# Optimization experiments

Measured on AMD Instinct MI355X. Metric: run time of the kernel, lower is better.

Reference implementation:

```python
import jax, jax.numpy as jnp
import numpy as np

N = 1000000
E = 16000000


def gcn_conv(x, W, b, src, dst, dinv_sqrt):
    # x: [N, Cin]; W: [Cin, Cout]; src/dst: [E'] (self-loops included)
    xw = x @ W                                   # [N, Cout]
    norm = dinv_sqrt[src] * dinv_sqrt[dst]       # [E']
    msg = xw[src] * norm[:, None]                # [E', Cout]
    out = jax.ops.segment_sum(msg, dst, num_segments=x.shape[0])
    return out + b


def setup_inputs() -> dict:
    key = jax.random.key(0)
    ks = jax.random.split(key, 8)
    x = jax.random.normal(ks[0], (N, 1), dtype=jnp.float32)
    edge_index = jax.random.randint(ks[1], (2, E), 0, N, dtype=jnp.int64)
    W1 = jax.random.normal(ks[2], (1, 3), dtype=jnp.float32)
    b1 = jax.random.normal(ks[3], (3,), dtype=jnp.float32) * 0.1
    W2 = jax.random.normal(ks[4], (3, 3), dtype=jnp.float32) * 0.5
    b2 = jax.random.normal(ks[5], (3,), dtype=jnp.float32) * 0.1
    W3 = jax.random.normal(ks[6], (3, 3), dtype=jnp.float32) * 0.5
    b3 = jax.random.normal(ks[7], (3,), dtype=jnp.float32) * 0.1
    return {"x": x, "edge_index": edge_index, "W1": W1, "b1": b1,
            "W2": W2, "b2": b2, "W3": W3, "b3": b3}


def reference(x, edge_index, W1, b1, W2, b2, W3, b3):
    n = x.shape[0]
    # add self-loops (PyG GCNConv default)
    loop = jnp.arange(n, dtype=edge_index.dtype)
    src = jnp.concatenate([edge_index[0], loop])
    dst = jnp.concatenate([edge_index[1], loop])
    # symmetric normalization: deg over targets of A + I
    deg = jax.ops.segment_sum(jnp.ones_like(dst, dtype=x.dtype), dst, num_segments=n)
    dinv_sqrt = jnp.where(deg > 0, jax.lax.rsqrt(deg), 0.0)
    h = jax.nn.relu(gcn_conv(x, W1, b1, src, dst, dinv_sqrt))
    h = jax.nn.relu(gcn_conv(h, W2, b2, src, dst, dinv_sqrt))
    h = jax.nn.relu(gcn_conv(h, W3, b3, src, dst, dinv_sqrt))
    return h
```

## Files before the change

kernel.cpp:

```cpp
#include <hip/hip_runtime.h>

#define THREADS 256
#define TILE 8192
#define TPB_S 512
#define EPT 16
#define BUCKET_BITS 10
#define BUCKET_SIZE 1024
#define NT_MAX 2048
#define STAGE_CAP 15616
#define MSK 0xFFFFFu

__device__ __forceinline__ long long llmin(long long a, long long b) { return a < b ? a : b; }


__global__ void detect_i64_kernel(const int* __restrict__ e, int* __restrict__ flag) {
    if (blockIdx.x == 0 && threadIdx.x == 0) {
        bool all_odd_zero = true, any_even = false;
#pragma unroll
        for (int k = 0; k < 16; ++k) {
            if (e[2 * k + 1] != 0) all_odd_zero = false;
            if (e[2 * k] != 0) any_even = true;
        }
        *flag = (all_odd_zero && any_even) ? 1 : 0;
    }
}


__global__ __launch_bounds__(TPB_S) void binsort_kernel(
        const int* __restrict__ e, long long E, const int* __restrict__ flag,
        int nbuck, int* __restrict__ packed, int* __restrict__ ofs) {
    __shared__ int hist[1024];
    __shared__ int sarr[TPB_S];
    __shared__ int srec[TILE];
    const int tid = threadIdx.x;
    hist[tid] = 0;
    hist[tid + TPB_S] = 0;
    __syncthreads();

    const bool i64 = (*flag != 0);
    const long long beg = (long long)blockIdx.x * TILE;
    const int tile_len = (int)llmin((long long)TILE, E - beg);

    int rec[EPT];
    int bkt[EPT];
#pragma unroll
    for (int k = 0; k < EPT; ++k) {
        int j = tid + k * TPB_S;
        bkt[k] = -1;
        if (j < tile_len) {
            long long idx = beg + j;
            int s, d;
            if (i64) { s = ((const int2*)e)[idx].x; d = ((const int2*)e)[E + idx].x; }
            else     { s = e[idx];                  d = e[E + idx]; }
            bkt[k] = d >> BUCKET_BITS;
            rec[k] = ((d & (BUCKET_SIZE - 1)) << 20) | s;
            atomicAdd(&hist[bkt[k]], 1);
        }
    }
    __syncthreads();

    int v0 = hist[2 * tid], v1 = hist[2 * tid + 1];
    sarr[tid] = v0 + v1;
    __syncthreads();
    for (int off = 1; off < TPB_S; off <<= 1) {
        int t = (tid >= off) ? sarr[tid - off] : 0;
        __syncthreads();
        sarr[tid] += t;
        __syncthreads();
    }
    int excl = (tid == 0) ? 0 : sarr[tid - 1];
    hist[2 * tid] = excl;
    hist[2 * tid + 1] = excl + v0;
    __syncthreads();

    int* orow = ofs + (size_t)blockIdx.x * nbuck;
    if (tid < nbuck) orow[tid] = hist[tid];
    if (tid + TPB_S < nbuck) orow[tid + TPB_S] = hist[tid + TPB_S];
    __syncthreads();

#pragma unroll
    for (int k = 0; k < EPT; ++k) {
        if (bkt[k] >= 0) {
            int pos = atomicAdd(&hist[bkt[k]], 1);
            srec[pos] = rec[k];
        }
    }
    __syncthreads();

    int* prow = packed + (size_t)blockIdx.x * TILE;
    for (int j = tid; j < tile_len; j += TPB_S) prow[j] = srec[j];
}

#define TRT 32
__global__ void transpose_kernel(const int* __restrict__ in, int rows, int cols,
                                 int* __restrict__ outT) {
    __shared__ int tb[TRT][TRT + 1];
    int c0 = blockIdx.x * TRT, r0 = blockIdx.y * TRT;
    int lx = threadIdx.x, ly = threadIdx.y;
    for (int dy = ly; dy < TRT; dy += 8) {
        int r = r0 + dy, c = c0 + lx;
        if (r < rows && c < cols) tb[dy][lx] = in[(size_t)r * cols + c];
    }
    __syncthreads();
    for (int dy = ly; dy < TRT; dy += 8) {
        int r = c0 + dy, c = r0 + lx;
        if (r < cols && c < rows) outT[(size_t)r * rows + c] = tb[lx][dy];
    }
}


__global__ __launch_bounds__(THREADS) void bcnt_kernel(
        const int* __restrict__ ofsT, long long E, int ntiles, int nbuck,
        int* __restrict__ bcnt) {
    __shared__ int sh[THREADS];
    const int b = blockIdx.x, tid = threadIdx.x;
    const int* row0 = ofsT + (size_t)b * ntiles;
    const int* row1 = row0 + ntiles;
    const bool last_b = (b == nbuck - 1);
    int s = 0;
    for (int t = tid; t < ntiles; t += THREADS) {
        int o = row0[t];
        int tl = (t == ntiles - 1) ? (int)(E - (long long)t * TILE) : TILE;
        int o2 = last_b ? tl : row1[t];
        s += o2 - o;
    }
    sh[tid] = s;
    __syncthreads();
    for (int off = THREADS >> 1; off > 0; off >>= 1) {
        if (tid < off) sh[tid] += sh[tid + off];
        __syncthreads();
    }
    if (tid == 0) bcnt[b] = sh[0];
}

__global__ __launch_bounds__(1024) void bscan_kernel(
        const int* __restrict__ bcnt, int nbuck, int* __restrict__ bs) {
    __shared__ int sh[1024];
    int tid = threadIdx.x;
    int v = (tid < nbuck) ? bcnt[tid] : 0;
    sh[tid] = v;
    __syncthreads();
    for (int off = 1; off < 1024; off <<= 1) {
        int t = (tid >= off) ? sh[tid - off] : 0;
        __syncthreads();
        sh[tid] += t;
        __syncthreads();
    }
    if (tid < nbuck) bs[tid] = sh[tid] - v;
    if (tid == nbuck - 1) bs[nbuck] = sh[tid];
}


__global__ __launch_bounds__(TPB_S) void merge_kernel(
        const int* __restrict__ ofsT, const int* __restrict__ packed,
        const int* __restrict__ bs, long long E, int ntiles, int nbuck,
        const float* __restrict__ x,
        int* __restrict__ merged, float* __restrict__ dinv, float* __restrict__ p,
        int N) {
    __shared__ int lofs[NT_MAX];
    __shared__ int tsum[TPB_S];
    __shared__ int stage[STAGE_CAP];
    __shared__ int cnt[BUCKET_SIZE];
    const int tid = threadIdx.x, b = blockIdx.x;
    const int* row0 = ofsT + (size_t)b * ntiles;
    const int* row1 = row0 + ntiles;
    const bool last_b = (b == nbuck - 1);
    const int per = (ntiles + TPB_S - 1) / TPB_S;
    const int t0 = tid * per;

    for (int k = tid; k < BUCKET_SIZE; k += TPB_S) cnt[k] = 0;

    int s = 0;
    for (int k = 0; k < per; ++k) {
        int t = t0 + k;
        if (t < ntiles) {
            int o = row0[t];
            int tl = (t == ntiles - 1) ? (int)(E - (long long)t * TILE) : TILE;
            int o2 = last_b ? tl : row1[t];
            lofs[t] = s;
            s += o2 - o;
        }
    }
    tsum[tid] = s;
    __syncthreads();
    for (int off = 1; off < TPB_S; off <<= 1) {
        int t = (tid >= off) ? tsum[tid - off] : 0;
        __syncthreads();
        tsum[tid] += t;
        __syncthreads();
    }
    const int excl = tsum[tid] - s;
    const int total = tsum[TPB_S - 1];
    for (int k = 0; k < per; ++k) {
        int t = t0 + k;
        if (t < ntiles) lofs[t] += excl;
    }
    __syncthreads();

    const int bsb = bs[b];
    for (int k = 0; k < per; ++k) {
        int t = t0 + k;
        if (t >= ntiles) break;
        int o = row0[t];
        int tl = (t == ntiles - 1) ? (int)(E - (long long)t * TILE) : TILE;
        int o2 = last_b ? tl : row1[t];
        const int* pr = packed + (size_t)t * TILE;
        int q = lofs[t];
        int j = o;
        for (; j + 4 <= o2; j += 4, q += 4) {
            int a0 = pr[j], a1 = pr[j + 1], a2 = pr[j + 2], a3 = pr[j + 3];
            atomicAdd(&cnt[((unsigned)a0) >> 20], 1);
            atomicAdd(&cnt[((unsigned)a1) >> 20], 1);
            atomicAdd(&cnt[((unsigned)a2) >> 20], 1);
            atomicAdd(&cnt[((unsigned)a3) >> 20], 1);
            if (q + 3 < STAGE_CAP) {
                stage[q] = a0; stage[q + 1] = a1; stage[q + 2] = a2; stage[q + 3] = a3;
            } else {
                if (q < STAGE_CAP) stage[q] = a0; else merged[bsb + q] = a0;
                if (q + 1 < STAGE_CAP) stage[q + 1] = a1; else merged[bsb + q + 1] = a1;
                if (q + 2 < STAGE_CAP) stage[q + 2] = a2; else merged[bsb + q + 2] = a2;
                merged[bsb + q + 3] = a3;
            }
        }
        for (; j < o2; ++j, ++q) {
            int a0 = pr[j];
            atomicAdd(&cnt[((unsigned)a0) >> 20], 1);
            if (q < STAGE_CAP) stage[q] = a0; else merged[bsb + q] = a0;
        }
    }
    __syncthreads();

    const int wlen = total < STAGE_CAP ? total : STAGE_CAP;
    for (int j = tid; j < wlen; j += TPB_S) merged[bsb + j] = stage[j];

    int nbase = b << BUCKET_BITS;
    for (int j = tid; j < BUCKET_SIZE; j += TPB_S) {
        int i = nbase + j;
        if (i < N) {
            float di = rsqrtf((float)cnt[j] + 1.0f);
            dinv[i] = di;
            p[i] = x[i] * di;
        }
    }
}


__global__ void layer1_bucket_kernel(const int* __restrict__ bs, const int* __restrict__ packed,
                                     const float* __restrict__ p, const float* __restrict__ dinv,
                                     const float* __restrict__ W1, const float* __restrict__ b1,
                                     const float* __restrict__ W2,
                                     float4* __restrict__ y2, int N) {
    __shared__ float acc[BUCKET_SIZE];
    for (int k = threadIdx.x; k < BUCKET_SIZE; k += blockDim.x) acc[k] = 0.0f;
    __syncthreads();
    int beg = bs[blockIdx.x], end = bs[blockIdx.x + 1];
    int stride = blockDim.x;
    int k = beg + threadIdx.x;
    for (; k + 3 * stride < end; k += 4 * stride) {
        unsigned r0 = packed[k], r1 = packed[k + stride];
        unsigned r2 = packed[k + 2 * stride], r3 = packed[k + 3 * stride];
        float v0 = p[r0 & MSK], v1 = p[r1 & MSK];
        float v2 = p[r2 & MSK], v3 = p[r3 & MSK];
        atomicAdd(&acc[r0 >> 20], v0);
        atomicAdd(&acc[r1 >> 20], v1);
        atomicAdd(&acc[r2 >> 20], v2);
        atomicAdd(&acc[r3 >> 20], v3);
    }
    for (; k < end; k += stride) {
        unsigned rec = (unsigned)packed[k];
        atomicAdd(&acc[rec >> 20], p[rec & MSK]);
    }
    __syncthreads();
    int base = blockIdx.x << BUCKET_BITS;
    for (int j = threadIdx.x; j < BUCKET_SIZE; j += blockDim.x) {
        int i = base + j;
        if (i >= N) continue;
        float di = dinv[i];
        float t = di * (acc[j] + p[i]);
        float h0 = fmaxf(t * W1[0] + b1[0], 0.0f);
        float h1 = fmaxf(t * W1[1] + b1[1], 0.0f);
        float h2 = fmaxf(t * W1[2] + b1[2], 0.0f);
        float4 o;
        o.x = di * (h0 * W2[0] + h1 * W2[3] + h2 * W2[6]);
        o.y = di * (h0 * W2[1] + h1 * W2[4] + h2 * W2[7]);
        o.z = di * (h0 * W2[2] + h1 * W2[5] + h2 * W2[8]);
        o.w = 0.0f;
        y2[i] = o;
    }
}

__global__ void layer_mid_bucket_kernel(const int* __restrict__ bs, const int* __restrict__ packed,
                                        const float4* __restrict__ y, const float* __restrict__ dinv,
                                        const float* __restrict__ b, const float* __restrict__ Wn,
                                        float4* __restrict__ ynext, int N) {
    __shared__ float acc[BUCKET_SIZE * 3];
    for (int k = threadIdx.x; k < BUCKET_SIZE * 3; k += blockDim.x) acc[k] = 0.0f;
    __syncthreads();
    int beg = bs[blockIdx.x], end = bs[blockIdx.x + 1];
    int stride = blockDim.x;
    int k = beg + threadIdx.x;
    for (; k + 3 * stride < end; k += 4 * stride) {
        unsigned r0 = packed[k], r1 = packed[k + stride];
        unsigned r2 = packed[k + 2 * stride], r3 = packed[k + 3 * stride];
        float4 v0 = y[r0 & MSK], v1 = y[r1 & MSK];
        float4 v2 = y[r2 & MSK], v3 = y[r3 & MSK];
        int d0 = (r0 >> 20) * 3, d1 = (r1 >> 20) * 3, d2 = (r2 >> 20) * 3, d3 = (r3 >> 20) * 3;
        atomicAdd(&acc[d0 + 0], v0.x); atomicAdd(&acc[d0 + 1], v0.y); atomicAdd(&acc[d0 + 2], v0.z);
        atomicAdd(&acc[d1 + 0], v1.x); atomicAdd(&acc[d1 + 1], v1.y); atomicAdd(&acc[d1 + 2], v1.z);
        atomicAdd(&acc[d2 + 0], v2.x); atomicAdd(&acc[d2 + 1], v2.y); atomicAdd(&acc[d2 + 2], v2.z);
        atomicAdd(&acc[d3 + 0], v3.x); atomicAdd(&acc[d3 + 1], v3.y); atomicAdd(&acc[d3 + 2], v3.z);
    }
    for (; k < end; k += stride) {
        unsigned rec = (unsigned)packed[k];
        float4 v = y[rec & MSK];
        int dl = (rec >> 20) * 3;
        atomicAdd(&acc[dl + 0], v.x);
        atomicAdd(&acc[dl + 1], v.y);
        atomicAdd(&acc[dl + 2], v.z);
    }
    __syncthreads();
    int base = blockIdx.x << BUCKET_BITS;
    for (int j = threadIdx.x; j < BUCKET_SIZE; j += blockDim.x) {
        int i = base + j;
        if (i >= N) continue;
        float di = dinv[i];
        float4 yi = y[i];
        float h0 = fmaxf(di * (acc[j * 3 + 0] + yi.x) + b[0], 0.0f);
        float h1 = fmaxf(di * (acc[j * 3 + 1] + yi.y) + b[1], 0.0f);
        float h2 = fmaxf(di * (acc[j * 3 + 2] + yi.z) + b[2], 0.0f);
        float4 o;
        o.x = di * (h0 * Wn[0] + h1 * Wn[3] + h2 * Wn[6]);
        o.y = di * (h0 * Wn[1] + h1 * Wn[4] + h2 * Wn[7]);
        o.z = di * (h0 * Wn[2] + h1 * Wn[5] + h2 * Wn[8]);
        o.w = 0.0f;
        ynext[i] = o;
    }
}

__global__ void layer_last_bucket_kernel(const int* __restrict__ bs, const int* __restrict__ packed,
                                         const float4* __restrict__ y, const float* __restrict__ dinv,
                                         const float* __restrict__ b,
                                         float* __restrict__ out, int N) {
    __shared__ float acc[BUCKET_SIZE * 3];
    for (int k = threadIdx.x; k < BUCKET_SIZE * 3; k += blockDim.x) acc[k] = 0.0f;
    __syncthreads();
    int beg = bs[blockIdx.x], end = bs[blockIdx.x + 1];
    int stride = blockDim.x;
    int k = beg + threadIdx.x;
    for (; k + 3 * stride < end; k += 4 * stride) {
        unsigned r0 = packed[k], r1 = packed[k + stride];
        unsigned r2 = packed[k + 2 * stride], r3 = packed[k + 3 * stride];
        float4 v0 = y[r0 & MSK], v1 = y[r1 & MSK];
        float4 v2 = y[r2 & MSK], v3 = y[r3 & MSK];
        int d0 = (r0 >> 20) * 3, d1 = (r1 >> 20) * 3, d2 = (r2 >> 20) * 3, d3 = (r3 >> 20) * 3;
        atomicAdd(&acc[d0 + 0], v0.x); atomicAdd(&acc[d0 + 1], v0.y); atomicAdd(&acc[d0 + 2], v0.z);
        atomicAdd(&acc[d1 + 0], v1.x); atomicAdd(&acc[d1 + 1], v1.y); atomicAdd(&acc[d1 + 2], v1.z);
        atomicAdd(&acc[d2 + 0], v2.x); atomicAdd(&acc[d2 + 1], v2.y); atomicAdd(&acc[d2 + 2], v2.z);
        atomicAdd(&acc[d3 + 0], v3.x); atomicAdd(&acc[d3 + 1], v3.y); atomicAdd(&acc[d3 + 2], v3.z);
    }
    for (; k < end; k += stride) {
        unsigned rec = (unsigned)packed[k];
        float4 v = y[rec & MSK];
        int dl = (rec >> 20) * 3;
        atomicAdd(&acc[dl + 0], v.x);
        atomicAdd(&acc[dl + 1], v.y);
        atomicAdd(&acc[dl + 2], v.z);
    }
    __syncthreads();
    int base = blockIdx.x << BUCKET_BITS;
    for (int j = threadIdx.x; j < BUCKET_SIZE; j += blockDim.x) {
        int i = base + j;
        if (i >= N) continue;
        float di = dinv[i];
        float4 yi = y[i];
        out[i * 3 + 0] = fmaxf(di * (acc[j * 3 + 0] + yi.x) + b[0], 0.0f);
        out[i * 3 + 1] = fmaxf(di * (acc[j * 3 + 1] + yi.y) + b[1], 0.0f);
        out[i * 3 + 2] = fmaxf(di * (acc[j * 3 + 2] + yi.z) + b[2], 0.0f);
    }
}


__global__ void deg_kernel(const int* __restrict__ e, long long E,
                           const int* __restrict__ flag, float* __restrict__ deg) {
    const bool i64 = (*flag != 0);
    long long i = (long long)blockIdx.x * blockDim.x + threadIdx.x;
    const long long stride = (long long)gridDim.x * blockDim.x;
    for (; i < E; i += stride) {
        long long t = i64 ? (long long)e[2 * E + 2 * i] : (long long)e[E + i];
        atomicAdd(deg + t, 1.0f);
    }
}

__global__ void node_init_kernel(const float* __restrict__ x, const float* __restrict__ W1,
                                 float* __restrict__ deg_dinv, float* __restrict__ A, int N) {
    int i = blockIdx.x * blockDim.x + threadIdx.x;
    if (i >= N) return;
    float di = rsqrtf(deg_dinv[i] + 1.0f);
    deg_dinv[i] = di;
    float v = x[i] * di;
    A[i * 3 + 0] = v * W1[0];
    A[i * 3 + 1] = v * W1[1];
    A[i * 3 + 2] = v * W1[2];
}

__global__ void scatter_kernel(const int* __restrict__ e, long long E,
                               const int* __restrict__ flag,
                               const float* __restrict__ y, float* __restrict__ acc) {
    const bool i64 = (*flag != 0);
    long long i = (long long)blockIdx.x * blockDim.x + threadIdx.x;
    const long long stride = (long long)gridDim.x * blockDim.x;
    for (; i < E; i += stride) {
        int s, t;
        if (i64) { s = e[2 * i]; t = e[2 * E + 2 * i]; }
        else     { s = e[i];     t = e[E + i]; }
        atomicAdd(acc + (long long)t * 3 + 0, y[(long long)s * 3 + 0]);
        atomicAdd(acc + (long long)t * 3 + 1, y[(long long)s * 3 + 1]);
        atomicAdd(acc + (long long)t * 3 + 2, y[(long long)s * 3 + 2]);
    }
}

__global__ void finalize_mid_kernel(const float* __restrict__ dinv, const float* __restrict__ y,
                                    float* __restrict__ acc, const float* __restrict__ b,
                                    const float* __restrict__ Wn, int N) {
    int i = blockIdx.x * blockDim.x + threadIdx.x;
    if (i >= N) return;
    float di = dinv[i];
    float h0 = fmaxf(di * (acc[i * 3 + 0] + y[i * 3 + 0]) + b[0], 0.0f);
    float h1 = fmaxf(di * (acc[i * 3 + 1] + y[i * 3 + 1]) + b[1], 0.0f);
    float h2 = fmaxf(di * (acc[i * 3 + 2] + y[i * 3 + 2]) + b[2], 0.0f);
    float z0 = di * (h0 * Wn[0] + h1 * Wn[3] + h2 * Wn[6]);
    float z1 = di * (h0 * Wn[1] + h1 * Wn[4] + h2 * Wn[7]);
    float z2 = di * (h0 * Wn[2] + h1 * Wn[5] + h2 * Wn[8]);
    acc[i * 3 + 0] = z0;
    acc[i * 3 + 1] = z1;
    acc[i * 3 + 2] = z2;
}

__global__ void finalize_last_kernel(const float* __restrict__ dinv, const float* __restrict__ y,
                                     const float* __restrict__ acc, const float* __restrict__ b,
                                     float* __restrict__ out, int N) {
    int i = blockIdx.x * blockDim.x + threadIdx.x;
    if (i >= N) return;
    float di = dinv[i];
    out[i * 3 + 0] = fmaxf(di * (acc[i * 3 + 0] + y[i * 3 + 0]) + b[0], 0.0f);
    out[i * 3 + 1] = fmaxf(di * (acc[i * 3 + 1] + y[i * 3 + 1]) + b[1], 0.0f);
    out[i * 3 + 2] = fmaxf(di * (acc[i * 3 + 2] + y[i * 3 + 2]) + b[2], 0.0f);
}


extern "C" void kernel_launch(void* const* d_in, const int* in_sizes, int n_in,
                              void* d_out, int out_size, void* d_ws, size_t ws_size,
                              hipStream_t stream) {
    const float* x  = (const float*)d_in[0];
    const int*   ei = (const int*)d_in[1];
    const float* W1 = (const float*)d_in[2];
    const float* b1 = (const float*)d_in[3];
    const float* W2 = (const float*)d_in[4];
    const float* b2 = (const float*)d_in[5];
    const float* W3 = (const float*)d_in[6];
    const float* b3 = (const float*)d_in[7];
    float* out = (float*)d_out;

    const long long N = in_sizes[0];
    const long long E = (long long)in_sizes[1] / 2;

    const int nbuck  = (int)((N + BUCKET_SIZE - 1) >> BUCKET_BITS);
    const int ntiles = (int)((E + TILE - 1) / TILE);

    char* w = (char*)d_ws;
    size_t off = 0;
    auto alloc = [&](size_t bytes) -> char* {
        char* pp = w + off;
        off = (off + bytes + 255) & ~(size_t)255;
        return pp;
    };

    int*    flag   = (int*)alloc(4);
    int*    ofs    = (int*)alloc((size_t)ntiles * nbuck * 4);
    int*    ofsT   = (int*)alloc((size_t)nbuck * ntiles * 4);
    int*    bcnt   = (int*)alloc((size_t)nbuck * 4);
    int*    bs     = (int*)alloc(((size_t)nbuck + 1) * 4);
    int*    packed = (int*)alloc((size_t)ntiles * TILE * 4);
    int*    merged = (int*)alloc((size_t)E * 4);
    float*  dinv   = (float*)alloc((size_t)N * 4);
    float*  p      = (float*)alloc((size_t)N * 4);
    float4* y2     = (float4*)packed;
    float4* y3     = (float4*)((char*)packed + (size_t)N * 16);

    const int nblk = (int)((N + THREADS - 1) / THREADS);

    if (off <= ws_size && N <= (1 << 20) && nbuck <= 1024 && ntiles <= NT_MAX &&
        (size_t)ntiles * TILE * 4 >= (size_t)N * 32) {
        detect_i64_kernel<<<1, 64, 0, stream>>>(ei, flag);
        binsort_kernel<<<ntiles, TPB_S, 0, stream>>>(ei, E, flag, nbuck, packed, ofs);
        dim3 tb(32, 8);
        dim3 tg((nbuck + TRT - 1) / TRT, (ntiles + TRT - 1) / TRT);
        transpose_kernel<<<tg, tb, 0, stream>>>(ofs, ntiles, nbuck, ofsT);
        bcnt_kernel<<<nbuck, THREADS, 0, stream>>>(ofsT, E, ntiles, nbuck, bcnt);
        bscan_kernel<<<1, 1024, 0, stream>>>(bcnt, nbuck, bs);
        merge_kernel<<<nbuck, TPB_S, 0, stream>>>(ofsT, packed, bs, E, ntiles, nbuck,
                                                  x, merged, dinv, p, (int)N);

        layer1_bucket_kernel<<<nbuck, THREADS, 0, stream>>>(bs, merged, p, dinv, W1, b1, W2, y2, (int)N);
        layer_mid_bucket_kernel<<<nbuck, THREADS, 0, stream>>>(bs, merged, y2, dinv, b2, W3, y3, (int)N);
        layer_last_bucket_kernel<<<nbuck, THREADS, 0, stream>>>(bs, merged, y3, dinv, b3, out, (int)N);
    } else {
        int*   fflag = (int*)w;
        float* fdinv = (float*)(w + 256);
        float* A     = fdinv + N;
        size_t need_full = 256 + (size_t)N * 4 + (size_t)N * 12 * 2;
        float* B = (ws_size >= need_full) ? (A + 3 * N) : out;
        const int eblk = 2048;

        detect_i64_kernel<<<1, 64, 0, stream>>>(ei, fflag);
        hipMemsetAsync(fdinv, 0, (size_t)N * 4, stream);
        deg_kernel<<<eblk, THREADS, 0, stream>>>(ei, E, fflag, fdinv);
        node_init_kernel<<<nblk, THREADS, 0, stream>>>(x, W1, fdinv, A, (int)N);

        hipMemsetAsync(B, 0, (size_t)N * 12, stream);
        scatter_kernel<<<eblk, THREADS, 0, stream>>>(ei, E, fflag, A, B);
        finalize_mid_kernel<<<nblk, THREADS, 0, stream>>>(fdinv, A, B, b1, W2, (int)N);

        hipMemsetAsync(A, 0, (size_t)N * 12, stream);
        scatter_kernel<<<eblk, THREADS, 0, stream>>>(ei, E, fflag, B, A);
        finalize_mid_kernel<<<nblk, THREADS, 0, stream>>>(fdinv, B, A, b2, W3, (int)N);

        hipMemsetAsync(B, 0, (size_t)N * 12, stream);
        scatter_kernel<<<eblk, THREADS, 0, stream>>>(ei, E, fflag, A, B);
        finalize_last_kernel<<<nblk, THREADS, 0, stream>>>(fdinv, A, B, b3, out, (int)N);
    }
}
```

Baseline: 763.4 us.

## Store hidden features as three planar arrays and gather per channel

Replaces the padded float4 node feature arrays with three separate float planes (SoA), and makes the mid and last layers run three passes over the bucket's edge list, one per channel, each gathering a single float. The aim is to shrink each random gather's working set from 16 MB to 4 MB per channel so it fits better in cache, and to drop the padding traffic. The cost is reading the packed edge list three times per layer and issuing three gathers per edge instead of one vector load.

```diff
diff --git a/kernel.cpp b/kernel.cpp
--- a/kernel.cpp
+++ b/kernel.cpp
@@ -245,11 +245,12 @@
 }
 
 
-__global__ void layer1_bucket_kernel(const int* __restrict__ bs, const int* __restrict__ packed,
+__global__ void layer1_bucket_kernel(const int* __restrict__ bs, const int* __restrict__ merged,
                                      const float* __restrict__ p, const float* __restrict__ dinv,
                                      const float* __restrict__ W1, const float* __restrict__ b1,
                                      const float* __restrict__ W2,
-                                     float4* __restrict__ y2, int N) {
+                                     float* __restrict__ Z0, float* __restrict__ Z1,
+                                     float* __restrict__ Z2, int N) {
     __shared__ float acc[BUCKET_SIZE];
     for (int k = threadIdx.x; k < BUCKET_SIZE; k += blockDim.x) acc[k] = 0.0f;
     __syncthreads();
@@ -257,8 +258,8 @@
     int stride = blockDim.x;
     int k = beg + threadIdx.x;
     for (; k + 3 * stride < end; k += 4 * stride) {
-        unsigned r0 = packed[k], r1 = packed[k + stride];
-        unsigned r2 = packed[k + 2 * stride], r3 = packed[k + 3 * stride];
+        unsigned r0 = merged[k], r1 = merged[k + stride];
+        unsigned r2 = merged[k + 2 * stride], r3 = merged[k + 3 * stride];
         float v0 = p[r0 & MSK], v1 = p[r1 & MSK];
         float v2 = p[r2 & MSK], v3 = p[r3 & MSK];
         atomicAdd(&acc[r0 >> 20], v0);
@@ -267,7 +268,7 @@
         atomicAdd(&acc[r3 >> 20], v3);
     }
     for (; k < end; k += stride) {
-        unsigned rec = (unsigned)packed[k];
+        unsigned rec = (unsigned)merged[k];
         atomicAdd(&acc[rec >> 20], p[rec & MSK]);
     }
     __syncthreads();
@@ -280,43 +281,44 @@
         float h0 = fmaxf(t * W1[0] + b1[0], 0.0f);
         float h1 = fmaxf(t * W1[1] + b1[1], 0.0f);
         float h2 = fmaxf(t * W1[2] + b1[2], 0.0f);
-        float4 o;
-        o.x = di * (h0 * W2[0] + h1 * W2[3] + h2 * W2[6]);
-        o.y = di * (h0 * W2[1] + h1 * W2[4] + h2 * W2[7]);
-        o.z = di * (h0 * W2[2] + h1 * W2[5] + h2 * W2[8]);
-        o.w = 0.0f;
-        y2[i] = o;
-    }
-}
-
-__global__ void layer_mid_bucket_kernel(const int* __restrict__ bs, const int* __restrict__ packed,
-                                        const float4* __restrict__ y, const float* __restrict__ dinv,
+        Z0[i] = di * (h0 * W2[0] + h1 * W2[3] + h2 * W2[6]);
+        Z1[i] = di * (h0 * W2[1] + h1 * W2[4] + h2 * W2[7]);
+        Z2[i] = di * (h0 * W2[2] + h1 * W2[5] + h2 * W2[8]);
+    }
+}
+
+
+__global__ void layer_mid_bucket_kernel(const int* __restrict__ bs, const int* __restrict__ merged,
+                                        const float* __restrict__ Y0, const float* __restrict__ Y1,
+                                        const float* __restrict__ Y2,
+                                        const float* __restrict__ dinv,
                                         const float* __restrict__ b, const float* __restrict__ Wn,
-                                        float4* __restrict__ ynext, int N) {
-    __shared__ float acc[BUCKET_SIZE * 3];
-    for (int k = threadIdx.x; k < BUCKET_SIZE * 3; k += blockDim.x) acc[k] = 0.0f;
+                                        float* __restrict__ Z0, float* __restrict__ Z1,
+                                        float* __restrict__ Z2, int N) {
+    __shared__ float acc[3 * BUCKET_SIZE];
+    for (int k = threadIdx.x; k < 3 * BUCKET_SIZE; k += blockDim.x) acc[k] = 0.0f;
     __syncthreads();
     int beg = bs[blockIdx.x], end = bs[blockIdx.x + 1];
     int stride = blockDim.x;
-    int k = beg + threadIdx.x;
-    for (; k + 3 * stride < end; k += 4 * stride) {
-        unsigned r0 = packed[k], r1 = packed[k + stride];
-        unsigned r2 = packed[k + 2 * stride], r3 = packed[k + 3 * stride];
-        float4 v0 = y[r0 & MSK], v1 = y[r1 & MSK];
-        float4 v2 = y[r2 & MSK], v3 = y[r3 & MSK];
-        int d0 = (r0 >> 20) * 3, d1 = (r1 >> 20) * 3, d2 = (r2 >> 20) * 3, d3 = (r3 >> 20) * 3;
-        atomicAdd(&acc[d0 + 0], v0.x); atomicAdd(&acc[d0 + 1], v0.y); atomicAdd(&acc[d0 + 2], v0.z);
-        atomicAdd(&acc[d1 + 0], v1.x); atomicAdd(&acc[d1 + 1], v1.y); atomicAdd(&acc[d1 + 2], v1.z);
-        atomicAdd(&acc[d2 + 0], v2.x); atomicAdd(&acc[d2 + 1], v2.y); atomicAdd(&acc[d2 + 2], v2.z);
-        atomicAdd(&acc[d3 + 0], v3.x); atomicAdd(&acc[d3 + 1], v3.y); atomicAdd(&acc[d3 + 2], v3.z);
-    }
-    for (; k < end; k += stride) {
-        unsigned rec = (unsigned)packed[k];
-        float4 v = y[rec & MSK];
-        int dl = (rec >> 20) * 3;
-        atomicAdd(&acc[dl + 0], v.x);
-        atomicAdd(&acc[dl + 1], v.y);
-        atomicAdd(&acc[dl + 2], v.z);
+#pragma unroll
+    for (int c = 0; c < 3; ++c) {
+        const float* Y = (c == 0) ? Y0 : (c == 1) ? Y1 : Y2;
+        float* ac = acc + c * BUCKET_SIZE;
+        int k = beg + threadIdx.x;
+        for (; k + 3 * stride < end; k += 4 * stride) {
+            unsigned r0 = merged[k], r1 = merged[k + stride];
+            unsigned r2 = merged[k + 2 * stride], r3 = merged[k + 3 * stride];
+            float v0 = Y[r0 & MSK], v1 = Y[r1 & MSK];
+            float v2 = Y[r2 & MSK], v3 = Y[r3 & MSK];
+            atomicAdd(&ac[r0 >> 20], v0);
+            atomicAdd(&ac[r1 >> 20], v1);
+            atomicAdd(&ac[r2 >> 20], v2);
+            atomicAdd(&ac[r3 >> 20], v3);
+        }
+        for (; k < end; k += stride) {
+            unsigned rec = (unsigned)merged[k];
+            atomicAdd(&ac[rec >> 20], Y[rec & MSK]);
+        }
     }
     __syncthreads();
     int base = blockIdx.x << BUCKET_BITS;
@@ -324,47 +326,45 @@
         int i = base + j;
         if (i >= N) continue;
         float di = dinv[i];
-        float4 yi = y[i];
-        float h0 = fmaxf(di * (acc[j * 3 + 0] + yi.x) + b[0], 0.0f);
-        float h1 = fmaxf(di * (acc[j * 3 + 1] + yi.y) + b[1], 0.0f);
-        float h2 = fmaxf(di * (acc[j * 3 + 2] + yi.z) + b[2], 0.0f);
-        float4 o;
-        o.x = di * (h0 * Wn[0] + h1 * Wn[3] + h2 * Wn[6]);
-        o.y = di * (h0 * Wn[1] + h1 * Wn[4] + h2 * Wn[7]);
-        o.z = di * (h0 * Wn[2] + h1 * Wn[5] + h2 * Wn[8]);
-        o.w = 0.0f;
-        ynext[i] = o;
-    }
-}
-
-__global__ void layer_last_bucket_kernel(const int* __restrict__ bs, const int* __restrict__ packed,
-                                         const float4* __restrict__ y, const float* __restrict__ dinv,
+        float h0 = fmaxf(di * (acc[j] + Y0[i]) + b[0], 0.0f);
+        float h1 = fmaxf(di * (acc[BUCKET_SIZE + j] + Y1[i]) + b[1], 0.0f);
+        float h2 = fmaxf(di * (acc[2 * BUCKET_SIZE + j] + Y2[i]) + b[2], 0.0f);
+        Z0[i] = di * (h0 * Wn[0] + h1 * Wn[3] + h2 * Wn[6]);
+        Z1[i] = di * (h0 * Wn[1] + h1 * Wn[4] + h2 * Wn[7]);
+        Z2[i] = di * (h0 * Wn[2] + h1 * Wn[5] + h2 * Wn[8]);
+    }
+}
+
+__global__ void layer_last_bucket_kernel(const int* __restrict__ bs, const int* __restrict__ merged,
+                                         const float* __restrict__ Y0, const float* __restrict__ Y1,
+                                         const float* __restrict__ Y2,
+                                         const float* __restrict__ dinv,
                                          const float* __restrict__ b,
                                          float* __restrict__ out, int N) {
-    __shared__ float acc[BUCKET_SIZE * 3];
-    for (int k = threadIdx.x; k < BUCKET_SIZE * 3; k += blockDim.x) acc[k] = 0.0f;
+    __shared__ float acc[3 * BUCKET_SIZE];
+    for (int k = threadIdx.x; k < 3 * BUCKET_SIZE; k += blockDim.x) acc[k] = 0.0f;
     __syncthreads();
     int beg = bs[blockIdx.x], end = bs[blockIdx.x + 1];
     int stride = blockDim.x;
-    int k = beg + threadIdx.x;
-    for (; k + 3 * stride < end; k += 4 * stride) {
-        unsigned r0 = packed[k], r1 = packed[k + stride];
-        unsigned r2 = packed[k + 2 * stride], r3 = packed[k + 3 * stride];
-        float4 v0 = y[r0 & MSK], v1 = y[r1 & MSK];
-        float4 v2 = y[r2 & MSK], v3 = y[r3 & MSK];
-        int d0 = (r0 >> 20) * 3, d1 = (r1 >> 20) * 3, d2 = (r2 >> 20) * 3, d3 = (r3 >> 20) * 3;
-        atomicAdd(&acc[d0 + 0], v0.x); atomicAdd(&acc[d0 + 1], v0.y); atomicAdd(&acc[d0 + 2], v0.z);
-        atomicAdd(&acc[d1 + 0], v1.x); atomicAdd(&acc[d1 + 1], v1.y); atomicAdd(&acc[d1 + 2], v1.z);
-        atomicAdd(&acc[d2 + 0], v2.x); atomicAdd(&acc[d2 + 1], v2.y); atomicAdd(&acc[d2 + 2], v2.z);
-        atomicAdd(&acc[d3 + 0], v3.x); atomicAdd(&acc[d3 + 1], v3.y); atomicAdd(&acc[d3 + 2], v3.z);
-    }
-    for (; k < end; k += stride) {
-        unsigned rec = (unsigned)packed[k];
-        float4 v = y[rec & MSK];
-        int dl = (rec >> 20) * 3;
-        atomicAdd(&acc[dl + 0], v.x);
-        atomicAdd(&acc[dl + 1], v.y);
-        atomicAdd(&acc[dl + 2], v.z);
+#pragma unroll
+    for (int c = 0; c < 3; ++c) {
+        const float* Y = (c == 0) ? Y0 : (c == 1) ? Y1 : Y2;
+        float* ac = acc + c * BUCKET_SIZE;
+        int k = beg + threadIdx.x;
+        for (; k + 3 * stride < end; k += 4 * stride) {
+            unsigned r0 = merged[k], r1 = merged[k + stride];
+            unsigned r2 = merged[k + 2 * stride], r3 = merged[k + 3 * stride];
+            float v0 = Y[r0 & MSK], v1 = Y[r1 & MSK];
+            float v2 = Y[r2 & MSK], v3 = Y[r3 & MSK];
+            atomicAdd(&ac[r0 >> 20], v0);
+            atomicAdd(&ac[r1 >> 20], v1);
+            atomicAdd(&ac[r2 >> 20], v2);
+            atomicAdd(&ac[r3 >> 20], v3);
+        }
+        for (; k < end; k += stride) {
+            unsigned rec = (unsigned)merged[k];
+            atomicAdd(&ac[rec >> 20], Y[rec & MSK]);
+        }
     }
     __syncthreads();
     int base = blockIdx.x << BUCKET_BITS;
@@ -372,10 +372,9 @@
         int i = base + j;
         if (i >= N) continue;
         float di = dinv[i];
-        float4 yi = y[i];
-        out[i * 3 + 0] = fmaxf(di * (acc[j * 3 + 0] + yi.x) + b[0], 0.0f);
-        out[i * 3 + 1] = fmaxf(di * (acc[j * 3 + 1] + yi.y) + b[1], 0.0f);
-        out[i * 3 + 2] = fmaxf(di * (acc[j * 3 + 2] + yi.z) + b[2], 0.0f);
+        out[i * 3 + 0] = fmaxf(di * (acc[j] + Y0[i]) + b[0], 0.0f);
+        out[i * 3 + 1] = fmaxf(di * (acc[BUCKET_SIZE + j] + Y1[i]) + b[1], 0.0f);
+        out[i * 3 + 2] = fmaxf(di * (acc[2 * BUCKET_SIZE + j] + Y2[i]) + b[2], 0.0f);
     }
 }
 
@@ -484,13 +483,17 @@
     int*    merged = (int*)alloc((size_t)E * 4);
     float*  dinv   = (float*)alloc((size_t)N * 4);
     float*  p      = (float*)alloc((size_t)N * 4);
-    float4* y2     = (float4*)packed;
-    float4* y3     = (float4*)((char*)packed + (size_t)N * 16);
+    float*  y2_0 = (float*)packed;
+    float*  y2_1 = y2_0 + N;
+    float*  y2_2 = y2_1 + N;
+    float*  y3_0 = y2_2 + N;
+    float*  y3_1 = y3_0 + N;
+    float*  y3_2 = y3_1 + N;
 
     const int nblk = (int)((N + THREADS - 1) / THREADS);
 
     if (off <= ws_size && N <= (1 << 20) && nbuck <= 1024 && ntiles <= NT_MAX &&
-        (size_t)ntiles * TILE * 4 >= (size_t)N * 32) {
+        (size_t)ntiles * TILE * 4 >= (size_t)N * 24) {
         detect_i64_kernel<<<1, 64, 0, stream>>>(ei, flag);
         binsort_kernel<<<ntiles, TPB_S, 0, stream>>>(ei, E, flag, nbuck, packed, ofs);
         dim3 tb(32, 8);
@@ -501,9 +504,13 @@
         merge_kernel<<<nbuck, TPB_S, 0, stream>>>(ofsT, packed, bs, E, ntiles, nbuck,
                                                   x, merged, dinv, p, (int)N);
 
-        layer1_bucket_kernel<<<nbuck, THREADS, 0, stream>>>(bs, merged, p, dinv, W1, b1, W2, y2, (int)N);
-        layer_mid_bucket_kernel<<<nbuck, THREADS, 0, stream>>>(bs, merged, y2, dinv, b2, W3, y3, (int)N);
-        layer_last_bucket_kernel<<<nbuck, THREADS, 0, stream>>>(bs, merged, y3, dinv, b3, out, (int)N);
+        layer1_bucket_kernel<<<nbuck, THREADS, 0, stream>>>(bs, merged, p, dinv, W1, b1, W2,
+                                                            y2_0, y2_1, y2_2, (int)N);
+        layer_mid_bucket_kernel<<<nbuck, THREADS, 0, stream>>>(bs, merged, y2_0, y2_1, y2_2,
+                                                               dinv, b2, W3,
+                                                               y3_0, y3_1, y3_2, (int)N);
+        layer_last_bucket_kernel<<<nbuck, THREADS, 0, stream>>>(bs, merged, y3_0, y3_1, y3_2,
+                                                                dinv, b3, out, (int)N);
     } else {
         int*   fflag = (int*)w;
         float* fdinv = (float*)(w + 256);
```

New measurement: 1.071 ms. 1.4x slower.

## Reorder bucket edges by source slice and gather slices in lockstep via grid sync

Applied to the files above, without the earlier changes.

Adds a pass that sorts each destination bucket's edges into 8 slices by source-node range, recording per-slice offsets. Layers 2 and 3 then run as cooperative kernels where all blocks handle the same source slice together and grid-sync between slices. The aim is to keep the randomly gathered y rows for the active slice resident in L2/LLC. The cost is the extra reorder kernel, eight grid-wide barriers per layer, and load imbalance across blocks at each barrier.

```diff
diff --git a/kernel.cpp b/kernel.cpp
--- a/kernel.cpp
+++ b/kernel.cpp
@@ -1,4 +1,7 @@
 #include <hip/hip_runtime.h>
+#include <hip/hip_cooperative_groups.h>
+
+namespace cg = cooperative_groups;
 
 #define THREADS 256
 #define TILE 8192
@@ -8,6 +11,9 @@
 #define BUCKET_SIZE 1024
 #define NT_MAX 2048
 #define STAGE_CAP 15616
+#define CAP2 16640
+#define NSLICE 8
+#define SLICE_SHIFT 17
 #define MSK 0xFFFFFu
 
 __device__ __forceinline__ long long llmin(long long a, long long b) { return a < b ? a : b; }
@@ -245,7 +251,68 @@
 }
 
 
-__global__ void layer1_bucket_kernel(const int* __restrict__ bs, const int* __restrict__ packed,
+__global__ __launch_bounds__(THREADS) void slice_reorder_kernel(
+        const int* __restrict__ bs, int* __restrict__ merged, int* __restrict__ sofs) {
+    __shared__ int stage2[CAP2];
+    __shared__ int f[NSLICE * THREADS];
+    __shared__ int sarr[THREADS];
+    const int b = blockIdx.x, tid = threadIdx.x;
+    const int base = bs[b];
+    const int len = bs[b + 1] - base;
+
+    if (len > CAP2) {
+        if (tid == 0) {
+            sofs[b * 9] = 0;
+            for (int s2 = 1; s2 <= NSLICE; ++s2) sofs[b * 9 + s2] = len;
+        }
+        return;
+    }
+
+    int c[NSLICE];
+#pragma unroll
+    for (int i = 0; i < NSLICE; ++i) c[i] = 0;
+    for (int j = tid; j < len; j += THREADS) {
+        unsigned r = (unsigned)merged[base + j];
+        c[(r & MSK) >> SLICE_SHIFT]++;
+    }
+#pragma unroll
+    for (int sl = 0; sl < NSLICE; ++sl) f[sl * THREADS + tid] = c[sl];
+    __syncthreads();
+
+    int loc[NSLICE];
+    int s = 0;
+#pragma unroll
+    for (int j = 0; j < NSLICE; ++j) { loc[j] = f[tid * NSLICE + j]; s += loc[j]; }
+    sarr[tid] = s;
+    __syncthreads();
+    for (int off = 1; off < THREADS; off <<= 1) {
+        int t = (tid >= off) ? sarr[tid - off] : 0;
+        __syncthreads();
+        sarr[tid] += t;
+        __syncthreads();
+    }
+    int ex = sarr[tid] - s;
+#pragma unroll
+    for (int j = 0; j < NSLICE; ++j) { f[tid * NSLICE + j] = ex; ex += loc[j]; }
+    __syncthreads();
+
+    int cur[NSLICE];
+#pragma unroll
+    for (int sl = 0; sl < NSLICE; ++sl) cur[sl] = f[sl * THREADS + tid];
+    if (tid < NSLICE) sofs[b * 9 + tid] = f[tid * THREADS];
+    if (tid == 0) sofs[b * 9 + NSLICE] = len;
+
+    for (int j = tid; j < len; j += THREADS) {
+        int r = merged[base + j];
+        int sl = (((unsigned)r) & MSK) >> SLICE_SHIFT;
+        stage2[cur[sl]++] = r;
+    }
+    __syncthreads();
+    for (int j = tid; j < len; j += THREADS) merged[base + j] = stage2[j];
+}
+
+
+__global__ void layer1_bucket_kernel(const int* __restrict__ bs, const int* __restrict__ merged,
                                      const float* __restrict__ p, const float* __restrict__ dinv,
                                      const float* __restrict__ W1, const float* __restrict__ b1,
                                      const float* __restrict__ W2,
@@ -257,8 +324,8 @@
     int stride = blockDim.x;
     int k = beg + threadIdx.x;
     for (; k + 3 * stride < end; k += 4 * stride) {
-        unsigned r0 = packed[k], r1 = packed[k + stride];
-        unsigned r2 = packed[k + 2 * stride], r3 = packed[k + 3 * stride];
+        unsigned r0 = merged[k], r1 = merged[k + stride];
+        unsigned r2 = merged[k + 2 * stride], r3 = merged[k + 3 * stride];
         float v0 = p[r0 & MSK], v1 = p[r1 & MSK];
         float v2 = p[r2 & MSK], v3 = p[r3 & MSK];
         atomicAdd(&acc[r0 >> 20], v0);
@@ -267,7 +334,7 @@
         atomicAdd(&acc[r3 >> 20], v3);
     }
     for (; k < end; k += stride) {
-        unsigned rec = (unsigned)packed[k];
+        unsigned rec = (unsigned)merged[k];
         atomicAdd(&acc[rec >> 20], p[rec & MSK]);
     }
     __syncthreads();
@@ -289,19 +356,13 @@
     }
 }
 
-__global__ void layer_mid_bucket_kernel(const int* __restrict__ bs, const int* __restrict__ packed,
-                                        const float4* __restrict__ y, const float* __restrict__ dinv,
-                                        const float* __restrict__ b, const float* __restrict__ Wn,
-                                        float4* __restrict__ ynext, int N) {
-    __shared__ float acc[BUCKET_SIZE * 3];
-    for (int k = threadIdx.x; k < BUCKET_SIZE * 3; k += blockDim.x) acc[k] = 0.0f;
-    __syncthreads();
-    int beg = bs[blockIdx.x], end = bs[blockIdx.x + 1];
-    int stride = blockDim.x;
+
+__device__ __forceinline__ void gather_slice(const int* merged, const float4* y,
+                                             float* acc, int beg, int end, int stride) {
     int k = beg + threadIdx.x;
     for (; k + 3 * stride < end; k += 4 * stride) {
-        unsigned r0 = packed[k], r1 = packed[k + stride];
-        unsigned r2 = packed[k + 2 * stride], r3 = packed[k + 3 * stride];
+        unsigned r0 = merged[k], r1 = merged[k + stride];
+        unsigned r2 = merged[k + 2 * stride], r3 = merged[k + 3 * stride];
         float4 v0 = y[r0 & MSK], v1 = y[r1 & MSK];
         float4 v2 = y[r2 & MSK], v3 = y[r3 & MSK];
         int d0 = (r0 >> 20) * 3, d1 = (r1 >> 20) * 3, d2 = (r2 >> 20) * 3, d3 = (r3 >> 20) * 3;
@@ -311,13 +372,93 @@
         atomicAdd(&acc[d3 + 0], v3.x); atomicAdd(&acc[d3 + 1], v3.y); atomicAdd(&acc[d3 + 2], v3.z);
     }
     for (; k < end; k += stride) {
-        unsigned rec = (unsigned)packed[k];
+        unsigned rec = (unsigned)merged[k];
         float4 v = y[rec & MSK];
         int dl = (rec >> 20) * 3;
         atomicAdd(&acc[dl + 0], v.x);
         atomicAdd(&acc[dl + 1], v.y);
         atomicAdd(&acc[dl + 2], v.z);
     }
+}
+
+__global__ __launch_bounds__(THREADS) void layer_mid_coop_kernel(
+        const int* __restrict__ bs, const int* __restrict__ sofs,
+        const int* __restrict__ merged,
+        const float4* __restrict__ y, const float* __restrict__ dinv,
+        const float* __restrict__ b, const float* __restrict__ Wn,
+        float4* __restrict__ ynext, int N) {
+    __shared__ float acc[BUCKET_SIZE * 3];
+    for (int k = threadIdx.x; k < BUCKET_SIZE * 3; k += blockDim.x) acc[k] = 0.0f;
+    __syncthreads();
+    cg::grid_group g = cg::this_grid();
+    const int bb = blockIdx.x;
+    const int base = bs[bb];
+    for (int s = 0; s < NSLICE; ++s) {
+        int beg = base + sofs[bb * 9 + s];
+        int end = base + sofs[bb * 9 + s + 1];
+        gather_slice(merged, y, acc, beg, end, blockDim.x);
+        g.sync();
+    }
+    __syncthreads();
+    int nbase = bb << BUCKET_BITS;
+    for (int j = threadIdx.x; j < BUCKET_SIZE; j += blockDim.x) {
+        int i = nbase + j;
+        if (i >= N) continue;
+        float di = dinv[i];
+        float4 yi = y[i];
+        float h0 = fmaxf(di * (acc[j * 3 + 0] + yi.x) + b[0], 0.0f);
+        float h1 = fmaxf(di * (acc[j * 3 + 1] + yi.y) + b[1], 0.0f);
+        float h2 = fmaxf(di * (acc[j * 3 + 2] + yi.z) + b[2], 0.0f);
+        float4 o;
+        o.x = di * (h0 * Wn[0] + h1 * Wn[3] + h2 * Wn[6]);
+        o.y = di * (h0 * Wn[1] + h1 * Wn[4] + h2 * Wn[7]);
+        o.z = di * (h0 * Wn[2] + h1 * Wn[5] + h2 * Wn[8]);
+        o.w = 0.0f;
+        ynext[i] = o;
+    }
+}
+
+__global__ __launch_bounds__(THREADS) void layer_last_coop_kernel(
+        const int* __restrict__ bs, const int* __restrict__ sofs,
+        const int* __restrict__ merged,
+        const float4* __restrict__ y, const float* __restrict__ dinv,
+        const float* __restrict__ b,
+        float* __restrict__ out, int N) {
+    __shared__ float acc[BUCKET_SIZE * 3];
+    for (int k = threadIdx.x; k < BUCKET_SIZE * 3; k += blockDim.x) acc[k] = 0.0f;
+    __syncthreads();
+    cg::grid_group g = cg::this_grid();
+    const int bb = blockIdx.x;
+    const int base = bs[bb];
+    for (int s = 0; s < NSLICE; ++s) {
+        int beg = base + sofs[bb * 9 + s];
+        int end = base + sofs[bb * 9 + s + 1];
+        gather_slice(merged, y, acc, beg, end, blockDim.x);
+        g.sync();
+    }
+    __syncthreads();
+    int nbase = bb << BUCKET_BITS;
+    for (int j = threadIdx.x; j < BUCKET_SIZE; j += blockDim.x) {
+        int i = nbase + j;
+        if (i >= N) continue;
+        float di = dinv[i];
+        float4 yi = y[i];
+        out[i * 3 + 0] = fmaxf(di * (acc[j * 3 + 0] + yi.x) + b[0], 0.0f);
+        out[i * 3 + 1] = fmaxf(di * (acc[j * 3 + 1] + yi.y) + b[1], 0.0f);
+        out[i * 3 + 2] = fmaxf(di * (acc[j * 3 + 2] + yi.z) + b[2], 0.0f);
+    }
+}
+
+
+__global__ void layer_mid_bucket_kernel(const int* __restrict__ bs, const int* __restrict__ merged,
+                                        const float4* __restrict__ y, const float* __restrict__ dinv,
+                                        const float* __restrict__ b, const float* __restrict__ Wn,
+                                        float4* __restrict__ ynext, int N) {
+    __shared__ float acc[BUCKET_SIZE * 3];
+    for (int k = threadIdx.x; k < BUCKET_SIZE * 3; k += blockDim.x) acc[k] = 0.0f;
+    __syncthreads();
+    int beg = bs[blockIdx.x], end = bs[blockIdx.x + 1];
+    gather_slice(merged, y, acc, beg, end, blockDim.x);
     __syncthreads();
     int base = blockIdx.x << BUCKET_BITS;
     for (int j = threadIdx.x; j < BUCKET_SIZE; j += blockDim.x) {
@@ -337,7 +478,7 @@
     }
 }
 
-__global__ void layer_last_bucket_kernel(const int* __restrict__ bs, const int* __restrict__ packed,
+__global__ void layer_last_bucket_kernel(const int* __restrict__ bs, const int* __restrict__ merged,
                                          const float4* __restrict__ y, const float* __restrict__ dinv,
                                          const float* __restrict__ b,
                                          float* __restrict__ out, int N) {
@@ -345,27 +486,7 @@
     for (int k = threadIdx.x; k < BUCKET_SIZE * 3; k += blockDim.x) acc[k] = 0.0f;
     __syncthreads();
     int beg = bs[blockIdx.x], end = bs[blockIdx.x + 1];
-    int stride = blockDim.x;
-    int k = beg + threadIdx.x;
-    for (; k + 3 * stride < end; k += 4 * stride) {
-        unsigned r0 = packed[k], r1 = packed[k + stride];
-        unsigned r2 = packed[k + 2 * stride], r3 = packed[k + 3 * stride];
-        float4 v0 = y[r0 & MSK], v1 = y[r1 & MSK];
-        float4 v2 = y[r2 & MSK], v3 = y[r3 & MSK];
-        int d0 = (r0 >> 20) * 3, d1 = (r1 >> 20) * 3, d2 = (r2 >> 20) * 3, d3 = (r3 >> 20) * 3;
-        atomicAdd(&acc[d0 + 0], v0.x); atomicAdd(&acc[d0 + 1], v0.y); atomicAdd(&acc[d0 + 2], v0.z);
-        atomicAdd(&acc[d1 + 0], v1.x); atomicAdd(&acc[d1 + 1], v1.y); atomicAdd(&acc[d1 + 2], v1.z);
-        atomicAdd(&acc[d2 + 0], v2.x); atomicAdd(&acc[d2 + 1], v2.y); atomicAdd(&acc[d2 + 2], v2.z);
-        atomicAdd(&acc[d3 + 0], v3.x); atomicAdd(&acc[d3 + 1], v3.y); atomicAdd(&acc[d3 + 2], v3.z);
-    }
-    for (; k < end; k += stride) {
-        unsigned rec = (unsigned)packed[k];
-        float4 v = y[rec & MSK];
-        int dl = (rec >> 20) * 3;
-        atomicAdd(&acc[dl + 0], v.x);
-        atomicAdd(&acc[dl + 1], v.y);
-        atomicAdd(&acc[dl + 2], v.z);
-    }
+    gather_slice(merged, y, acc, beg, end, blockDim.x);
     __syncthreads();
     int base = blockIdx.x << BUCKET_BITS;
     for (int j = threadIdx.x; j < BUCKET_SIZE; j += blockDim.x) {
@@ -480,6 +601,7 @@
     int*    ofsT   = (int*)alloc((size_t)nbuck * ntiles * 4);
     int*    bcnt   = (int*)alloc((size_t)nbuck * 4);
     int*    bs     = (int*)alloc(((size_t)nbuck + 1) * 4);
+    int*    sofs   = (int*)alloc((size_t)nbuck * 9 * 4);
     int*    packed = (int*)alloc((size_t)ntiles * TILE * 4);
     int*    merged = (int*)alloc((size_t)E * 4);
     float*  dinv   = (float*)alloc((size_t)N * 4);
@@ -500,10 +622,31 @@
         bscan_kernel<<<1, 1024, 0, stream>>>(bcnt, nbuck, bs);
         merge_kernel<<<nbuck, TPB_S, 0, stream>>>(ofsT, packed, bs, E, ntiles, nbuck,
                                                   x, merged, dinv, p, (int)N);
+        slice_reorder_kernel<<<nbuck, THREADS, 0, stream>>>(bs, merged, sofs);
 
         layer1_bucket_kernel<<<nbuck, THREADS, 0, stream>>>(bs, merged, p, dinv, W1, b1, W2, y2, (int)N);
-        layer_mid_bucket_kernel<<<nbuck, THREADS, 0, stream>>>(bs, merged, y2, dinv, b2, W3, y3, (int)N);
-        layer_last_bucket_kernel<<<nbuck, THREADS, 0, stream>>>(bs, merged, y3, dinv, b3, out, (int)N);
+
+        int Ni = (int)N;
+        const int* bs_p = bs; const int* sofs_p = sofs; const int* mg_p = merged;
+        const float* dinv_p = dinv;
+        const float4* y2_p = y2; float4* y3_p = y3;
+        const float* b2_p = b2; const float* W3_p = W3;
+        void* argsM[] = {(void*)&bs_p, (void*)&sofs_p, (void*)&mg_p, (void*)&y2_p,
+                         (void*)&dinv_p, (void*)&b2_p, (void*)&W3_p, (void*)&y3_p, (void*)&Ni};
+        hipError_t ec = hipLaunchCooperativeKernel((void*)layer_mid_coop_kernel,
+                                                   dim3(nbuck), dim3(THREADS), argsM, 0, stream);
+        if (ec != hipSuccess) {
+            layer_mid_bucket_kernel<<<nbuck, THREADS, 0, stream>>>(bs, merged, y2, dinv, b2, W3, y3, (int)N);
+        }
+
+        const float4* y3c_p = y3; const float* b3_p = b3; float* out_p = out;
+        void* argsL[] = {(void*)&bs_p, (void*)&sofs_p, (void*)&mg_p, (void*)&y3c_p,
+                         (void*)&dinv_p, (void*)&b3_p, (void*)&out_p, (void*)&Ni};
+        hipError_t ec2 = hipLaunchCooperativeKernel((void*)layer_last_coop_kernel,
+                                                    dim3(nbuck), dim3(THREADS), argsL, 0, stream);
+        if (ec2 != hipSuccess) {
+            layer_last_bucket_kernel<<<nbuck, THREADS, 0, stream>>>(bs, merged, y3, dinv, b3, out, (int)N);
+        }
     } else {
         int*   fflag = (int*)w;
         float* fdinv = (float*)(w + 256);
```

Result: slower. 2.650 ms (+247.1%).
